# Optimization experiments

Hardware: AMD Instinct MI355X
Metric: run time of the kernel (lower is better)

## Reference

```python
import jax, jax.numpy as jnp
import numpy as np

EPS = 1e-3        # Sinkhorn regularization (SinkhornDistance default)
MAX_ITER = 10     # max Sinkhorn iterations
THRESH = 0.1      # early-stop threshold on |u - u_prev|
N, P, D = 8, 2048, 64


def _l2norm(x):
    # F.normalize(x, dim=-1): x / max(||x||_2, 1e-12)
    return x / jnp.maximum(jnp.linalg.norm(x, axis=-1, keepdims=True), 1e-12)


def _l1norm(x):
    # F.normalize(x, p=1, dim=-1)
    return x / jnp.maximum(jnp.sum(jnp.abs(x), axis=-1, keepdims=True), 1e-12)


def _M(C, u, v):
    # modified cost M_ij = (-C_ij + u_i + v_j) / eps
    return (-C + u[..., :, None] + v[..., None, :]) / EPS


def _sinkhorn_uv(C, mu, nu):
    """Log-domain Sinkhorn with early stopping (matches torch loop + err.item() break)."""
    u0 = jnp.zeros_like(mu)
    v0 = jnp.zeros_like(nu)

    def cond(st):
        i, u, v, err = st
        return jnp.logical_and(i < MAX_ITER, err >= THRESH)

    def body(st):
        i, u, v, _ = st
        u1 = u
        u = EPS * (jnp.log(mu + 1e-8) - jax.nn.logsumexp(_M(C, u, v), axis=-1)) + u
        # logsumexp of M^T over last dim == logsumexp of M over axis -2
        v = EPS * (jnp.log(nu + 1e-8) - jax.nn.logsumexp(_M(C, u, v), axis=-2)) + v
        err = jnp.mean(jnp.sum(jnp.abs(u - u1), axis=-1))
        return (i + 1, u, v, err)

    _, u, v, _ = jax.lax.while_loop(
        cond, body, (jnp.int32(0), u0, v0, jnp.float32(jnp.inf)))
    return u, v


def setup_inputs() -> dict:
    key = jax.random.key(0)
    ka, kb = jax.random.split(key)
    a = jax.random.normal(ka, (N, P, D), dtype=jnp.float32)
    b = jax.random.normal(kb, (N, P, D), dtype=jnp.float32)
    return {"a": a, "b": b}


def reference(a, b):
    a = _l2norm(a)
    b = _l2norm(b)
    cost = 1.0 - jnp.einsum('bnd,bmd->bnm', a, b)          # [N, P1, P2]

    # weights computed from detached cost
    Cd = jax.lax.stop_gradient(cost)
    S = 1.0 - Cd
    wa = _l1norm(jnp.clip(_l1norm(jnp.mean(S, axis=2)), 0.0))  # [N, P1]
    wb = _l1norm(jnp.clip(_l1norm(jnp.mean(S, axis=1)), 0.0))  # [N, P2]

    u, v = _sinkhorn_uv(Cd, wa, wb)
    pi = jax.lax.stop_gradient(jnp.exp(_M(Cd, u, v)))       # transport plan, detached
    D_out = jnp.sum(pi * cost, axis=(-2, -1))               # [N], reduction='none'
    return D_out
```

## Files before the change

### kernel.cpp

```cpp
#include <hip/hip_runtime.h>
#include <math.h>

#define NB 8
#define PP 2048
#define DD 64
#define EPSF 1e-3f
#define RCPE 1000.0f
#define TMAX 10
#define THRESHF 0.1f
#define NEG_INF (-1e30f)
#define QSCALE 32767.5f
#define S_DEQ  (1.0f / 32767.5f)
#define KR 512
#define KC 512
#define TSEL 0.15f
#define TSELQ 4915

typedef __attribute__((ext_vector_type(8))) short bf16x8;
typedef __attribute__((ext_vector_type(4))) float f32x4;

__device__ __forceinline__ float waveAllMax(float v) {
#pragma unroll
    for (int m = 1; m < 64; m <<= 1) v = fmaxf(v, __shfl_xor(v, m, 64));
    return v;
}
__device__ __forceinline__ int waveAllMinI(int v) {
#pragma unroll
    for (int m = 1; m < 64; m <<= 1) v = min(v, __shfl_xor(v, m, 64));
    return v;
}
__device__ __forceinline__ float waveAllSum(float v) {
#pragma unroll
    for (int m = 1; m < 64; m <<= 1) v += __shfl_xor(v, m, 64);
    return v;
}
__device__ __forceinline__ short f2bf(float x) {
    unsigned b = __float_as_uint(x);
    return (short)((b + 0x7FFFu + ((b >> 16) & 1u)) >> 16);
}
__device__ __forceinline__ float bf2f(short h) {
    return __uint_as_float(((unsigned)(unsigned short)h) << 16);
}
__device__ __forceinline__ unsigned pknorm_u16(float a, float b) {
    unsigned r;
    asm("v_cvt_pknorm_u16_f32 %0, %1, %2" : "=v"(r) : "v"(a), "v"(b));
    return r;
}

__global__ void norm_kernel(const float* __restrict__ a, const float* __restrict__ b,
                            short* __restrict__ ahi, short* __restrict__ alo,
                            short* __restrict__ bhi, short* __restrict__ blo,
                            float* __restrict__ u, float* __restrict__ v,
                            int* __restrict__ conv, float* __restrict__ out,
                            float* __restrict__ Sa) {
    int gt = blockIdx.x * 256 + threadIdx.x;
    if (gt < NB * PP) { u[gt] = 0.0f; v[gt] = 0.0f; }
    if (gt == 0) *conv = 0;
    if (gt < NB) out[gt] = 0.0f;
    if (gt < 2 * NB * DD) Sa[gt] = 0.0f;
    int wave = gt >> 6;
    int lane = threadIdx.x & 63;
    const float* src; short* dhi; short* dlo; int row;
    if (wave < NB * PP) { src = a; dhi = ahi; dlo = alo; row = wave; }
    else                { src = b; dhi = bhi; dlo = blo; row = wave - NB * PP; }
    float x = src[(size_t)row * DD + lane];
    float ss = waveAllSum(x * x);
    float r = 1.0f / fmaxf(sqrtf(ss), 1e-12f);
    float xn = x * r;
    short h = f2bf(xn);
    dhi[(size_t)row * DD + lane] = h;
    dlo[(size_t)row * DD + lane] = f2bf(xn - bf2f(h));
}

__global__ void sumvec_kernel(const short* __restrict__ ahi, const short* __restrict__ alo,
                              const short* __restrict__ bhi, const short* __restrict__ blo,
                              float* __restrict__ Sa, float* __restrict__ Sb) {
    int b = blockIdx.x >> 3;
    bool isB = (blockIdx.x >> 2) & 1;
    int qtr = blockIdx.x & 3;
    const short* hi = (isB ? bhi : ahi) + ((size_t)b * PP + qtr * 512) * DD;
    const short* lo = (isB ? blo : alo) + ((size_t)b * PP + qtr * 512) * DD;
    float* dst = (isB ? Sb : Sa) + b * DD;
    int t = threadIdx.x;
    int w = t >> 6, lane = t & 63;
    int rl = lane >> 3, dq = lane & 7;
    float s[8] = {};
#pragma unroll
    for (int it = 0; it < 16; ++it) {
        size_t o = (size_t)(w * 128 + it * 8 + rl) * DD + dq * 8;
        bf16x8 h = *(const bf16x8*)(hi + o);
        bf16x8 l = *(const bf16x8*)(lo + o);
#pragma unroll
        for (int e = 0; e < 8; ++e) s[e] += bf2f(h[e]) + bf2f(l[e]);
    }
#pragma unroll
    for (int e = 0; e < 8; ++e) {
#pragma unroll
        for (int m = 8; m < 64; m <<= 1) s[e] += __shfl_xor(s[e], m, 64);
    }
    __shared__ float sh[4][64];
    if (rl == 0) {
#pragma unroll
        for (int e = 0; e < 8; ++e) sh[w][dq * 8 + e] = s[e];
    }
    __syncthreads();
    if (t < 64) atomicAdd(&dst[t], sh[0][t] + sh[1][t] + sh[2][t] + sh[3][t]);
}

__global__ __launch_bounds__(256, 4) void cost_kernel(const short* __restrict__ ahi,
        const short* __restrict__ alo, const short* __restrict__ bhi,
        const short* __restrict__ blo, unsigned short* __restrict__ C16,
        unsigned* __restrict__ rminp, unsigned* __restrict__ cminp) {
    __shared__ short Bs[2][128 * 64];
    __shared__ unsigned cmin2[4][128];
    int b  = blockIdx.z;
    int i0 = blockIdx.y * 128;
    int j0 = blockIdx.x * 128;
    int t = threadIdx.x, w = t >> 6, lane = t & 63;
    int quad = lane >> 4, li = lane & 15;
    const char* bh = (const char*)(bhi + ((size_t)b * PP + j0) * DD);
    const char* bl = (const char*)(blo + ((size_t)b * PP + j0) * DD);
    uint4 st[8];
#pragma unroll
    for (int i = 0; i < 4; ++i) {
        unsigned x = (unsigned)(t + i * 256) * 16;
        unsigned sx = x ^ (((x >> 7) & 7u) << 4);
        st[i]     = *(const uint4*)(bh + sx);
        st[4 + i] = *(const uint4*)(bl + sx);
    }
#pragma unroll
    for (int i = 0; i < 4; ++i) {
        unsigned x = (unsigned)(t + i * 256) * 16;
        *(uint4*)((char*)&Bs[0][0] + x) = st[i];
        *(uint4*)((char*)&Bs[1][0] + x) = st[4 + i];
    }
    __syncthreads();
    size_t Aoff = ((size_t)b * PP + i0 + w * 32) * DD;
    f32x4 acc[2][2][4] = {};
#pragma unroll
    for (int kc = 0; kc < 2; ++kc) {
        int k0 = kc * 32 + quad * 8;
        bf16x8 fah[2], fal[2];
#pragma unroll
        for (int mt = 0; mt < 2; ++mt) {
            size_t o = Aoff + (size_t)(mt * 16 + li) * DD + k0;
            fah[mt] = *(const bf16x8*)(ahi + o);
            fal[mt] = *(const bf16x8*)(alo + o);
        }
#pragma unroll
        for (int nh = 0; nh < 2; ++nh) {
#pragma unroll
            for (int ntl = 0; ntl < 4; ++ntl) {
                int col = nh * 64 + li * 4 + ntl;
                unsigned xo = ((unsigned)col * 128 + (unsigned)(kc * 4 + quad) * 16)
                              ^ (((unsigned)col & 7u) << 4);
                bf16x8 fbh = *(const bf16x8*)((const char*)&Bs[0][0] + xo);
                bf16x8 fbl = *(const bf16x8*)((const char*)&Bs[1][0] + xo);
#pragma unroll
                for (int mt = 0; mt < 2; ++mt) {
                    acc[mt][nh][ntl] = __builtin_amdgcn_mfma_f32_16x16x32_bf16(
                            fah[mt], fbh, acc[mt][nh][ntl], 0, 0, 0);
                    acc[mt][nh][ntl] = __builtin_amdgcn_mfma_f32_16x16x32_bf16(
                            fah[mt], fbl, acc[mt][nh][ntl], 0, 0, 0);
                    acc[mt][nh][ntl] = __builtin_amdgcn_mfma_f32_16x16x32_bf16(
                            fal[mt], fbh, acc[mt][nh][ntl], 0, 0, 0);
                }
            }
        }
    }
    unsigned cmin[2][4] = {{0xFFFFFFFFu, 0xFFFFFFFFu, 0xFFFFFFFFu, 0xFFFFFFFFu},
                           {0xFFFFFFFFu, 0xFFFFFFFFu, 0xFFFFFFFFu, 0xFFFFFFFFu}};
#pragma unroll
    for (int mt = 0; mt < 2; ++mt) {
#pragma unroll
        for (int r = 0; r < 4; ++r) {
            int irow = w * 32 + mt * 16 + quad * 4 + r;
            unsigned rm = 0xFFFFFFFFu;
            unsigned rowkey = (unsigned)(i0 + irow);
#pragma unroll
            for (int nh = 0; nh < 2; ++nh) {
                float f0 = fmaf(acc[mt][nh][0][r], -0.5f, 0.5f);
                float f1 = fmaf(acc[mt][nh][1][r], -0.5f, 0.5f);
                float f2 = fmaf(acc[mt][nh][2][r], -0.5f, 0.5f);
                float f3 = fmaf(acc[mt][nh][3][r], -0.5f, 0.5f);
                unsigned w0 = pknorm_u16(f0, f1);
                unsigned w1 = pknorm_u16(f2, f3);
                uint2 pv; pv.x = w0; pv.y = w1;
                *(uint2*)&C16[((size_t)b * PP + i0 + irow) * PP + j0 + nh * 64 + li * 4] = pv;
                unsigned colb = (unsigned)(j0 + nh * 64 + li * 4);
                unsigned lo0 = w0 << 16, hi0 = w0 & 0xFFFF0000u;
                unsigned lo1 = w1 << 16, hi1 = w1 & 0xFFFF0000u;
                rm = min(rm, min(min(lo0 | colb, hi0 | (colb + 1)),
                                 min(lo1 | (colb + 2), hi1 | (colb + 3))));
                cmin[nh][0] = min(cmin[nh][0], lo0 | rowkey);
                cmin[nh][1] = min(cmin[nh][1], hi0 | rowkey);
                cmin[nh][2] = min(cmin[nh][2], lo1 | rowkey);
                cmin[nh][3] = min(cmin[nh][3], hi1 | rowkey);
            }
#pragma unroll
            for (int m = 1; m < 16; m <<= 1)
                rm = min(rm, (unsigned)__shfl_xor((int)rm, m, 64));
            if (li == 0)
                rminp[(size_t)blockIdx.x * (NB * PP) + b * PP + i0 + irow] = rm;
        }
    }
#pragma unroll
    for (int nh = 0; nh < 2; ++nh) {
#pragma unroll
        for (int ntl = 0; ntl < 4; ++ntl) {
            unsigned cmv = cmin[nh][ntl];
            cmv = min(cmv, (unsigned)__shfl_xor((int)cmv, 16, 64));
            cmv = min(cmv, (unsigned)__shfl_xor((int)cmv, 32, 64));
            if (quad == 0) cmin2[w][nh * 64 + li * 4 + ntl] = cmv;
        }
    }
    __syncthreads();
    if (t < 128)
        cminp[(size_t)blockIdx.y * (NB * PP) + b * PP + j0 + t] =
            min(min(cmin2[0][t], cmin2[1][t]), min(cmin2[2][t], cmin2[3][t]));
}

__global__ void combine_kernel(const unsigned* __restrict__ rminp,
                               const unsigned* __restrict__ cminp,
                               unsigned* __restrict__ rowminp, unsigned* __restrict__ colminp) {
    int idx = blockIdx.x * 256 + threadIdx.x;
    unsigned rm = 0xFFFFFFFFu, cm = 0xFFFFFFFFu;
#pragma unroll
    for (int k = 0; k < 16; ++k)
        rm = min(rm, rminp[(size_t)k * (NB * PP) + idx]);
#pragma unroll
    for (int k = 0; k < 16; ++k)
        cm = min(cm, cminp[(size_t)k * (NB * PP) + idx]);
    rowminp[idx] = rm; colminp[idx] = cm;
}

__device__ __forceinline__ float blockReduceSum256(float v, float* sh) {
    v = waveAllSum(v);
    int lane = threadIdx.x & 63, w = threadIdx.x >> 6;
    if (lane == 0) sh[w] = v;
    __syncthreads();
    float r = sh[0] + sh[1] + sh[2] + sh[3];
    __syncthreads();
    return r;
}

__global__ void weights_kernel(const float* __restrict__ Sa, const float* __restrict__ Sb,
                               const short* __restrict__ ahi, const short* __restrict__ alo,
                               const short* __restrict__ bhi, const short* __restrict__ blo,
                               const unsigned* __restrict__ rowminp, const unsigned* __restrict__ colminp,
                               float* __restrict__ elm, float* __restrict__ eln,
                               unsigned short* __restrict__ rowminq,
                               unsigned short* __restrict__ colminq,
                               unsigned short* __restrict__ cthq) {
    __shared__ float sh[4];
    __shared__ float sv[64];
    int b = blockIdx.x & 7;
    bool isB = blockIdx.x >= 8;
    const short* hi = (isB ? bhi : ahi) + (size_t)b * PP * DD;
    const short* lo = (isB ? blo : alo) + (size_t)b * PP * DD;
    const float* svecg = (isB ? Sa : Sb) + b * DD;
    float* dst = (isB ? eln : elm) + b * PP;
    int tid = threadIdx.x;
    if (tid < 64) sv[tid] = svecg[tid];
    __syncthreads();
    float x[8];
    float sabs = 0.0f;
#pragma unroll
    for (int q = 0; q < 8; ++q) {
        int row = tid + q * 256;
        float dot = 0.0f;
#pragma unroll
        for (int dq = 0; dq < 8; ++dq) {
            bf16x8 h = *(const bf16x8*)(hi + (size_t)row * DD + dq * 8);
            bf16x8 l = *(const bf16x8*)(lo + (size_t)row * DD + dq * 8);
#pragma unroll
            for (int e = 0; e < 8; ++e)
                dot += (bf2f(h[e]) + bf2f(l[e])) * sv[dq * 8 + e];
        }
        x[q] = dot * (1.0f / (float)PP);
        sabs += fabsf(x[q]);
    }
    sabs = blockReduceSum256(sabs, sh);
    float inv1 = 1.0f / fmaxf(sabs, 1e-12f);
    float spos = 0.0f;
#pragma unroll
    for (int q = 0; q < 8; ++q) {
        x[q] = fmaxf(x[q] * inv1, 0.0f);
        spos += x[q];
    }
    spos = blockReduceSum256(spos, sh);
    float inv2 = 1.0f / fmaxf(spos, 1e-12f);
#pragma unroll
    for (int q = 0; q < 8; ++q)
        dst[tid + q * 256] = EPSF * logf(x[q] * inv2 + 1e-8f);
    if (isB) {
#pragma unroll
        for (int q = 0; q < 8; ++q) {
            int idx = b * PP + tid + q * 256;
            unsigned pc = colminp[idx];
            unsigned arg = pc & 0xffffu;
            unsigned pr = rowminp[b * PP + arg];
            colminq[idx] = (unsigned short)(pc >> 16);
            cthq[idx] = (unsigned short)((pc >> 16) - (pr >> 16));
        }
    } else {
#pragma unroll
        for (int q = 0; q < 8; ++q) {
            int idx = b * PP + tid + q * 256;
            rowminq[idx] = (unsigned short)(rowminp[idx] >> 16);
        }
    }
}

__global__ __launch_bounds__(256) void select_kernel(const unsigned short* __restrict__ C16,
        const unsigned short* __restrict__ colminq, const unsigned short* __restrict__ rowminq,
        const unsigned short* __restrict__ cthq,
        unsigned* __restrict__ rlist, int* __restrict__ rcnt,
        unsigned* __restrict__ clist, int* __restrict__ scnt) {
    __shared__ unsigned tile32[64][36];
    __shared__ int rm_s[64];
    __shared__ unsigned lcnt[64];
    if (blockIdx.x < 4096) {
        int w = threadIdx.x >> 6, lane = threadIdx.x & 63;
        int row = blockIdx.x * 4 + w;
        int b = row >> 11;
        const uint4* cp = (const uint4*)(C16 + (size_t)row * PP);
        uint4 q4[4];
#pragma unroll
        for (int g = 0; g < 4; ++g) q4[g] = cp[g * 64 + lane];
        const unsigned short* cmb = colminq + b * PP;
        int d[32];
        int rpmin = 0x7FFFFFFF;
#pragma unroll
        for (int g = 0; g < 4; ++g) {
            int jb = g * 512 + lane * 8;
            uint4 cmw = *(const uint4*)(cmb + jb);
            unsigned cw[4] = {cmw.x, cmw.y, cmw.z, cmw.w};
            unsigned qq[4] = {q4[g].x, q4[g].y, q4[g].z, q4[g].w};
#pragma unroll
            for (int h = 0; h < 4; ++h) {
                int d0 = (int)(qq[h] & 0xffffu) - (int)(cw[h] & 0xffffu);
                int d1 = (int)(qq[h] >> 16)     - (int)(cw[h] >> 16);
                d[g * 8 + h * 2]     = d0;
                d[g * 8 + h * 2 + 1] = d1;
                rpmin = min(rpmin, min(d0, d1));
            }
        }
        int rth = waveAllMinI(rpmin) + TSELQ;
        int cnt = 0;
#pragma unroll
        for (int e = 0; e < 32; ++e) cnt += (d[e] <= rth) ? 1 : 0;
        int inc = cnt;
#pragma unroll
        for (int m = 1; m < 64; m <<= 1) {
            int t2 = __shfl_up(inc, m, 64);
            if (lane >= m) inc += t2;
        }
        int p = inc - cnt;
        unsigned* rl = rlist + (size_t)row * KR;
#pragma unroll
        for (int g = 0; g < 4; ++g) {
            int jb = g * 512 + lane * 8;
            unsigned qq[4] = {q4[g].x, q4[g].y, q4[g].z, q4[g].w};
#pragma unroll
            for (int e = 0; e < 8; ++e) {
                if (d[g * 8 + e] <= rth) {
                    unsigned q = (qq[e >> 1] >> ((e & 1) * 16)) & 0xffffu;
                    if (p < KR) rl[p] = ((unsigned)(jb + e) << 16) | q;
                    ++p;
                }
            }
        }
        if (lane == 63) rcnt[row] = inc;
    } else {
        int bid = blockIdx.x - 4096;
        int b = bid >> 7;
        int rem = bid & 127;
        int j0 = (rem >> 2) * 64;
        int r0 = (rem & 3) * 512;
        int qq = rem & 3;
        int t = threadIdx.x;
        int col = t & 63, seg = t >> 6;
        int ctj = (int)cthq[b * PP + j0 + col] + TSELQ;
        unsigned* mylist = clist + ((size_t)(b * PP + j0 + col)) * KC + qq * 128;
        if (t < 64) lcnt[t] = 0;
        int lrow = t >> 3, lcc = t & 7;
        uint4 pf0, pf1; int pfr = 0;
        {
            const unsigned short* base0 = C16 + ((size_t)b * PP + r0 + lrow) * PP + j0;
            pf0 = ((const uint4*)base0)[lcc];
            pf1 = ((const uint4*)(base0 + (size_t)32 * PP))[lcc];
            if (t < 64) pfr = (int)rowminq[b * PP + r0 + t];
        }
        for (int chunk = 0; chunk < 8; ++chunk) {
            *(uint4*)&tile32[lrow][lcc * 4]      = pf0;
            *(uint4*)&tile32[32 + lrow][lcc * 4] = pf1;
            if (t < 64) rm_s[t] = pfr;
            __syncthreads();
            if (chunk < 7) {
                int rn = r0 + (chunk + 1) * 64;
                const unsigned short* base0 = C16 + ((size_t)b * PP + rn + lrow) * PP + j0;
                pf0 = ((const uint4*)base0)[lcc];
                pf1 = ((const uint4*)(base0 + (size_t)32 * PP))[lcc];
                if (t < 64) pfr = (int)rowminq[b * PP + rn + t];
            }
            int rbase = r0 + chunk * 64;
            unsigned qv[16];
            unsigned mask16 = 0;
            int sel = 0;
#pragma unroll
            for (int rr = 0; rr < 16; ++rr) {
                int rowl = seg * 16 + rr;
                unsigned w32 = tile32[rowl][col >> 1];
                unsigned q = (col & 1) ? (w32 >> 16) : (w32 & 0xffffu);
                qv[rr] = q;
                if ((int)q - rm_s[rowl] <= ctj) { mask16 |= 1u << rr; ++sel; }
            }
            unsigned basep = sel ? atomicAdd(&lcnt[col], (unsigned)sel) : 0u;
#pragma unroll
            for (int rr = 0; rr < 16; ++rr) {
                if (mask16 & (1u << rr)) {
                    if (basep < 128)
                        mylist[basep] = ((unsigned)(rbase + seg * 16 + rr) << 16) | qv[rr];
                    ++basep;
                }
            }
            __syncthreads();
        }
        if (t < 64)
            scnt[(b * PP + j0 + t) * 4 + qq] = min((int)lcnt[t], 128);
    }
}

__global__ __launch_bounds__(512) void u_kernel(const unsigned* __restrict__ rlist,
        const int* __restrict__ rcnt, const float* __restrict__ v,
        const float* __restrict__ elm, float* __restrict__ u, float* __restrict__ du,
        const int* __restrict__ conv) {
    if (*conv) return;
    int g = threadIdx.x >> 4, l = threadIdx.x & 15;
    int row = blockIdx.x * 32 + g;
    int b = row >> 11;
    int cnt = min(rcnt[row], KR);
    const unsigned* lst = rlist + (size_t)row * KR;
    const float* vb = v + (b << 11);
    float m = NEG_INF;
    for (int e = l; e < cnt; e += 16) {
        unsigned wd = lst[e];
        m = fmaxf(m, vb[wd >> 16] - (float)(wd & 0xffffu) * S_DEQ);
    }
#pragma unroll
    for (int mm = 1; mm < 16; mm <<= 1) m = fmaxf(m, __shfl_xor(m, mm, 64));
    float s = 0.0f;
    for (int e = l; e < cnt; e += 16) {
        unsigned wd = lst[e];
        float x = vb[wd >> 16] - (float)(wd & 0xffffu) * S_DEQ;
        s += __expf((x - m) * RCPE);
    }
#pragma unroll
    for (int mm = 1; mm < 16; mm <<= 1) s += __shfl_xor(s, mm, 64);
    if (l == 0) {
        float un = elm[row] - m - EPSF * logf(s);
        du[row] = fabsf(un - u[row]);
        u[row] = un;
    }
}

__global__ __launch_bounds__(512) void v_kernel(const unsigned* __restrict__ clist,
        const int* __restrict__ scnt, const float* __restrict__ u,
        const float* __restrict__ eln, float* __restrict__ v,
        const float* __restrict__ du, int* __restrict__ conv) {
    if (*conv) return;
    int g = threadIdx.x >> 4, l = threadIdx.x & 15;
    int jg = blockIdx.x * 32 + g;
    int b = jg >> 11;
    int4 sc = *(const int4*)&scnt[jg * 4];
    int cn[4] = {sc.x, sc.y, sc.z, sc.w};
    const unsigned* lst = clist + (size_t)jg * KC;
    const float* ub = u + (b << 11);
    float m = NEG_INF;
#pragma unroll
    for (int sg = 0; sg < 4; ++sg) {
        for (int k = l; k < cn[sg]; k += 16) {
            unsigned wd = lst[sg * 128 + k];
            m = fmaxf(m, ub[wd >> 16] - (float)(wd & 0xffffu) * S_DEQ);
        }
    }
#pragma unroll
    for (int mm = 1; mm < 16; mm <<= 1) m = fmaxf(m, __shfl_xor(m, mm, 64));
    float s = 0.0f;
#pragma unroll
    for (int sg = 0; sg < 4; ++sg) {
        for (int k = l; k < cn[sg]; k += 16) {
            unsigned wd = lst[sg * 128 + k];
            float x = ub[wd >> 16] - (float)(wd & 0xffffu) * S_DEQ;
            s += __expf((x - m) * RCPE);
        }
    }
#pragma unroll
    for (int mm = 1; mm < 16; mm <<= 1) s += __shfl_xor(s, mm, 64);
    if (l == 0)
        v[jg] = eln[jg] - m - EPSF * logf(s);
    if (blockIdx.x == 0) {
        __shared__ float sh[8];
        int t = threadIdx.x;
        int w = t >> 6, lane = t & 63;
        float sacc = 0.0f;
#pragma unroll
        for (int q = 0; q < 32; ++q) sacc += du[t + q * 512];
        sacc = waveAllSum(sacc);
        if (lane == 0) sh[w] = sacc;
        __syncthreads();
        if (t == 0) {
            float tot = sh[0] + sh[1] + sh[2] + sh[3] + sh[4] + sh[5] + sh[6] + sh[7];
            if (tot * (1.0f / (float)NB) < THRESHF) *conv = 1;
        }
    }
}

__global__ __launch_bounds__(512) void emd_kernel(const unsigned* __restrict__ rlist,
        const int* __restrict__ rcnt, const float* __restrict__ u,
        const float* __restrict__ v, float* __restrict__ epart) {
    __shared__ float sh[8];
    int g = threadIdx.x >> 4, l = threadIdx.x & 15;
    int row = blockIdx.x * 32 + g;
    int b = row >> 11;
    int cnt = min(rcnt[row], KR);
    const unsigned* lst = rlist + (size_t)row * KR;
    const float* vb = v + (b << 11);
    float ui = u[row];
    float s = 0.0f;
    for (int e = l; e < cnt; e += 16) {
        unsigned wd = lst[e];
        float cf = (float)(wd & 0xffffu) * S_DEQ;
        s += __expf((ui + vb[wd >> 16] - cf) * RCPE) * cf;
    }
    s = waveAllSum(s);
    int w = threadIdx.x >> 6, lane = threadIdx.x & 63;
    if (lane == 0) sh[w] = s;
    __syncthreads();
    if (threadIdx.x == 0)
        epart[blockIdx.x] = sh[0] + sh[1] + sh[2] + sh[3] + sh[4] + sh[5] + sh[6] + sh[7];
}

__global__ void emd_finalize(const float* __restrict__ epart,
                             float* __restrict__ out) {
    int b = blockIdx.x, l = threadIdx.x;
    float s = epart[b * 64 + l];
    s = waveAllSum(s);
    if (l == 0) out[b] = s;
}

extern "C" void kernel_launch(void* const* d_in, const int* in_sizes, int n_in,
                              void* d_out, int out_size, void* d_ws, size_t ws_size,
                              hipStream_t stream) {
    const float* a = (const float*)d_in[0];
    const float* b = (const float*)d_in[1];
    float* out = (float*)d_out;

    const size_t MBs = 1024ull * 1024ull;
    char* ws = (char*)d_ws;
    unsigned short* C16 = (unsigned short*)ws;
    short* ahi   = (short*)(ws + 64 * MBs);
    short* alo   = (short*)(ws + 66 * MBs);
    short* bhi   = (short*)(ws + 68 * MBs);
    short* blo   = (short*)(ws + 70 * MBs);
    unsigned* rminp = (unsigned*)(ws + 72 * MBs);
    unsigned* cminp = (unsigned*)(ws + 74 * MBs);
    unsigned* rlist = (unsigned*)(ws + 64 * MBs);
    unsigned* clist = (unsigned*)(ws + 96 * MBs);
    char* tail = ws + 128 * MBs;
    size_t off = 0;
    const size_t szV = (size_t)NB * PP * 4;
    const size_t szH = (size_t)NB * PP * 2;
    int*   scnt    = (int*)(tail + off); off += (size_t)NB * PP * 4 * 4;
    unsigned* rowminp = (unsigned*)(tail + off); off += szV;
    unsigned* colminp = (unsigned*)(tail + off); off += szV;
    unsigned short* rowminq = (unsigned short*)(tail + off); off += szH;
    unsigned short* colminq = (unsigned short*)(tail + off); off += szH;
    unsigned short* cthq    = (unsigned short*)(tail + off); off += szH;
    float* elm     = (float*)(tail + off); off += szV;
    float* eln     = (float*)(tail + off); off += szV;
    float* u       = (float*)(tail + off); off += szV;
    float* v       = (float*)(tail + off); off += szV;
    float* du      = (float*)(tail + off); off += szV;
    int*   rcnt    = (int*)(tail + off); off += szV;
    float* Sa      = (float*)(tail + off); off += (size_t)2 * NB * DD * 4;
    float* Sb      = Sa + NB * DD;
    float* epart   = (float*)(tail + off); off += (size_t)512 * 4;
    int*   conv    = (int*)(tail + off); off += 64;
    if (ws_size < 128 * MBs + off) return;

    norm_kernel<<<(2 * NB * PP) / 4, 256, 0, stream>>>(a, b, ahi, alo, bhi, blo,
            u, v, conv, out, Sa);
    sumvec_kernel<<<64, 256, 0, stream>>>(ahi, alo, bhi, blo, Sa, Sb);
    cost_kernel<<<dim3(PP / 128, PP / 128, NB), 256, 0, stream>>>(
            ahi, alo, bhi, blo, C16, rminp, cminp);
    combine_kernel<<<64, 256, 0, stream>>>(rminp, cminp, rowminp, colminp);
    weights_kernel<<<16, 256, 0, stream>>>(Sa, Sb, ahi, alo, bhi, blo,
            rowminp, colminp, elm, eln, rowminq, colminq, cthq);
    select_kernel<<<4096 + 1024, 256, 0, stream>>>(C16, colminq, rowminq,
            cthq, rlist, rcnt, clist, scnt);
    for (int it = 0; it < TMAX; ++it) {
        u_kernel<<<NB * PP / 32, 512, 0, stream>>>(rlist, rcnt, v, elm, u, du, conv);
        v_kernel<<<NB * PP / 32, 512, 0, stream>>>(clist, scnt, u, eln, v, du, conv);
    }
    emd_kernel<<<NB * PP / 32, 512, 0, stream>>>(rlist, rcnt, u, v, epart);
    emd_finalize<<<NB, 64, 0, stream>>>(epart, out);
}
```

Before: 351.1 us.

## Fuse Sinkhorn iterations and EMD into one persistent kernel with grid barriers

Replaces the 20 separate u/v kernel launches plus the EMD and finalize kernels with a single persistent kernel of 128 blocks. The blocks synchronize through atomic-counter grid barriers, and convergence is checked in-kernel so the loop exits early. The aim is to remove per-launch overhead and the idle tail of many small kernels. In exchange, only 128 blocks run, each handling 4 rows per 16-lane group, so parallelism drops. Spin barriers also rely on all blocks being co-resident.

```diff
diff --git a/kernel.cpp b/kernel.cpp
--- a/kernel.cpp
+++ b/kernel.cpp
@@ -15,6 +15,7 @@
 #define KC 512
 #define TSEL 0.15f
 #define TSELQ 4915
+#define SBLK 128
 
 typedef __attribute__((ext_vector_type(8))) short bf16x8;
 typedef __attribute__((ext_vector_type(4))) float f32x4;
@@ -45,6 +46,18 @@
     unsigned r;
     asm("v_cvt_pknorm_u16_f32 %0, %1, %2" : "=v"(r) : "v"(a), "v"(b));
     return r;
+}
+__device__ __forceinline__ void gridBarrier(int* cnt, int target) {
+    __syncthreads();
+    if (threadIdx.x == 0) {
+        __threadfence();
+        atomicAdd(cnt, 1);
+        while (__hip_atomic_load(cnt, __ATOMIC_RELAXED,
+                                 __HIP_MEMORY_SCOPE_AGENT) < target)
+            __builtin_amdgcn_s_sleep(8);
+        __threadfence();
+    }
+    __syncthreads();
 }
 
 __global__ void norm_kernel(const float* __restrict__ a, const float* __restrict__ b,
@@ -52,12 +65,13 @@
                             short* __restrict__ bhi, short* __restrict__ blo,
                             float* __restrict__ u, float* __restrict__ v,
                             int* __restrict__ conv, float* __restrict__ out,
-                            float* __restrict__ Sa) {
+                            float* __restrict__ Sa, int* __restrict__ bars) {
     int gt = blockIdx.x * 256 + threadIdx.x;
     if (gt < NB * PP) { u[gt] = 0.0f; v[gt] = 0.0f; }
     if (gt == 0) *conv = 0;
     if (gt < NB) out[gt] = 0.0f;
     if (gt < 2 * NB * DD) Sa[gt] = 0.0f;
+    if (gt < 64) bars[gt] = 0;
     int wave = gt >> 6;
     int lane = threadIdx.x & 63;
     const float* src; short* dhi; short* dlo; int row;
@@ -432,122 +446,124 @@
     }
 }
 
-__global__ __launch_bounds__(512) void u_kernel(const unsigned* __restrict__ rlist,
-        const int* __restrict__ rcnt, const float* __restrict__ v,
-        const float* __restrict__ elm, float* __restrict__ u, float* __restrict__ du,
-        const int* __restrict__ conv) {
-    if (*conv) return;
-    int g = threadIdx.x >> 4, l = threadIdx.x & 15;
-    int row = blockIdx.x * 32 + g;
-    int b = row >> 11;
-    int cnt = min(rcnt[row], KR);
-    const unsigned* lst = rlist + (size_t)row * KR;
-    const float* vb = v + (b << 11);
-    float m = NEG_INF;
-    for (int e = l; e < cnt; e += 16) {
-        unsigned wd = lst[e];
-        m = fmaxf(m, vb[wd >> 16] - (float)(wd & 0xffffu) * S_DEQ);
-    }
-#pragma unroll
-    for (int mm = 1; mm < 16; mm <<= 1) m = fmaxf(m, __shfl_xor(m, mm, 64));
+__global__ __launch_bounds__(512) void sinkhorn_kernel(
+        const unsigned* __restrict__ rlist, const int* __restrict__ rcnt,
+        const unsigned* __restrict__ clist, const int* __restrict__ scnt,
+        const float* __restrict__ elm, const float* __restrict__ eln,
+        float* __restrict__ u, float* __restrict__ v,
+        float* __restrict__ du, float* __restrict__ epart,
+        float* __restrict__ out, int* __restrict__ conv, int* __restrict__ bars) {
+    int t = threadIdx.x;
+    int g = t >> 4, l = t & 15;
+    int blk = blockIdx.x;
+    int bi = 0;
+    __shared__ float sh[8];
+    for (int it = 0; it < TMAX; ++it) {
+#pragma unroll
+        for (int k = 0; k < 4; ++k) {
+            int row = blk * 128 + g * 4 + k;
+            int b = row >> 11;
+            int cnt = min(rcnt[row], KR);
+            const unsigned* lst = rlist + (size_t)row * KR;
+            const float* vb = v + (b << 11);
+            float m = NEG_INF;
+            for (int e = l; e < cnt; e += 16) {
+                unsigned wd = lst[e];
+                m = fmaxf(m, vb[wd >> 16] - (float)(wd & 0xffffu) * S_DEQ);
+            }
+#pragma unroll
+            for (int mm = 1; mm < 16; mm <<= 1) m = fmaxf(m, __shfl_xor(m, mm, 64));
+            float s = 0.0f;
+            for (int e = l; e < cnt; e += 16) {
+                unsigned wd = lst[e];
+                s += __expf((vb[wd >> 16] - (float)(wd & 0xffffu) * S_DEQ - m) * RCPE);
+            }
+#pragma unroll
+            for (int mm = 1; mm < 16; mm <<= 1) s += __shfl_xor(s, mm, 64);
+            if (l == 0) {
+                float un = elm[row] - m - EPSF * logf(s);
+                du[row] = fabsf(un - u[row]);
+                u[row] = un;
+            }
+        }
+        gridBarrier(&bars[bi++], SBLK);
+        if (blk == 0) {
+            float sacc = 0.0f;
+#pragma unroll
+            for (int q = 0; q < 32; ++q) sacc += du[t + q * 512];
+            sacc = waveAllSum(sacc);
+            if ((t & 63) == 0) sh[t >> 6] = sacc;
+            __syncthreads();
+            if (t == 0) {
+                float tot = sh[0] + sh[1] + sh[2] + sh[3] + sh[4] + sh[5] + sh[6] + sh[7];
+                if (tot * (1.0f / (float)NB) < THRESHF)
+                    __hip_atomic_store(conv, 1, __ATOMIC_RELAXED,
+                                       __HIP_MEMORY_SCOPE_AGENT);
+            }
+            __syncthreads();
+        }
+#pragma unroll
+        for (int k = 0; k < 4; ++k) {
+            int jg = blk * 128 + g * 4 + k;
+            int b = jg >> 11;
+            int4 sc = *(const int4*)&scnt[jg * 4];
+            int cn[4] = {sc.x, sc.y, sc.z, sc.w};
+            const unsigned* lst = clist + (size_t)jg * KC;
+            const float* ub = u + (b << 11);
+            float m = NEG_INF;
+#pragma unroll
+            for (int sg = 0; sg < 4; ++sg) {
+                for (int kk = l; kk < cn[sg]; kk += 16) {
+                    unsigned wd = lst[sg * 128 + kk];
+                    m = fmaxf(m, ub[wd >> 16] - (float)(wd & 0xffffu) * S_DEQ);
+                }
+            }
+#pragma unroll
+            for (int mm = 1; mm < 16; mm <<= 1) m = fmaxf(m, __shfl_xor(m, mm, 64));
+            float s = 0.0f;
+#pragma unroll
+            for (int sg = 0; sg < 4; ++sg) {
+                for (int kk = l; kk < cn[sg]; kk += 16) {
+                    unsigned wd = lst[sg * 128 + kk];
+                    s += __expf((ub[wd >> 16] - (float)(wd & 0xffffu) * S_DEQ - m) * RCPE);
+                }
+            }
+#pragma unroll
+            for (int mm = 1; mm < 16; mm <<= 1) s += __shfl_xor(s, mm, 64);
+            if (l == 0)
+                v[jg] = eln[jg] - m - EPSF * logf(s);
+        }
+        gridBarrier(&bars[bi++], SBLK);
+        if (__hip_atomic_load(conv, __ATOMIC_RELAXED, __HIP_MEMORY_SCOPE_AGENT))
+            break;
+    }
     float s = 0.0f;
-    for (int e = l; e < cnt; e += 16) {
-        unsigned wd = lst[e];
-        float x = vb[wd >> 16] - (float)(wd & 0xffffu) * S_DEQ;
-        s += __expf((x - m) * RCPE);
-    }
-#pragma unroll
-    for (int mm = 1; mm < 16; mm <<= 1) s += __shfl_xor(s, mm, 64);
-    if (l == 0) {
-        float un = elm[row] - m - EPSF * logf(s);
-        du[row] = fabsf(un - u[row]);
-        u[row] = un;
-    }
-}
-
-__global__ __launch_bounds__(512) void v_kernel(const unsigned* __restrict__ clist,
-        const int* __restrict__ scnt, const float* __restrict__ u,
-        const float* __restrict__ eln, float* __restrict__ v,
-        const float* __restrict__ du, int* __restrict__ conv) {
-    if (*conv) return;
-    int g = threadIdx.x >> 4, l = threadIdx.x & 15;
-    int jg = blockIdx.x * 32 + g;
-    int b = jg >> 11;
-    int4 sc = *(const int4*)&scnt[jg * 4];
-    int cn[4] = {sc.x, sc.y, sc.z, sc.w};
-    const unsigned* lst = clist + (size_t)jg * KC;
-    const float* ub = u + (b << 11);
-    float m = NEG_INF;
-#pragma unroll
-    for (int sg = 0; sg < 4; ++sg) {
-        for (int k = l; k < cn[sg]; k += 16) {
-            unsigned wd = lst[sg * 128 + k];
-            m = fmaxf(m, ub[wd >> 16] - (float)(wd & 0xffffu) * S_DEQ);
-        }
-    }
-#pragma unroll
-    for (int mm = 1; mm < 16; mm <<= 1) m = fmaxf(m, __shfl_xor(m, mm, 64));
-    float s = 0.0f;
-#pragma unroll
-    for (int sg = 0; sg < 4; ++sg) {
-        for (int k = l; k < cn[sg]; k += 16) {
-            unsigned wd = lst[sg * 128 + k];
-            float x = ub[wd >> 16] - (float)(wd & 0xffffu) * S_DEQ;
-            s += __expf((x - m) * RCPE);
-        }
-    }
-#pragma unroll
-    for (int mm = 1; mm < 16; mm <<= 1) s += __shfl_xor(s, mm, 64);
-    if (l == 0)
-        v[jg] = eln[jg] - m - EPSF * logf(s);
-    if (blockIdx.x == 0) {
-        __shared__ float sh[8];
-        int t = threadIdx.x;
-        int w = t >> 6, lane = t & 63;
-        float sacc = 0.0f;
-#pragma unroll
-        for (int q = 0; q < 32; ++q) sacc += du[t + q * 512];
-        sacc = waveAllSum(sacc);
-        if (lane == 0) sh[w] = sacc;
-        __syncthreads();
-        if (t == 0) {
-            float tot = sh[0] + sh[1] + sh[2] + sh[3] + sh[4] + sh[5] + sh[6] + sh[7];
-            if (tot * (1.0f / (float)NB) < THRESHF) *conv = 1;
-        }
-    }
-}
-
-__global__ __launch_bounds__(512) void emd_kernel(const unsigned* __restrict__ rlist,
-        const int* __restrict__ rcnt, const float* __restrict__ u,
-        const float* __restrict__ v, float* __restrict__ epart) {
-    __shared__ float sh[8];
-    int g = threadIdx.x >> 4, l = threadIdx.x & 15;
-    int row = blockIdx.x * 32 + g;
-    int b = row >> 11;
-    int cnt = min(rcnt[row], KR);
-    const unsigned* lst = rlist + (size_t)row * KR;
-    const float* vb = v + (b << 11);
-    float ui = u[row];
-    float s = 0.0f;
-    for (int e = l; e < cnt; e += 16) {
-        unsigned wd = lst[e];
-        float cf = (float)(wd & 0xffffu) * S_DEQ;
-        s += __expf((ui + vb[wd >> 16] - cf) * RCPE) * cf;
+#pragma unroll
+    for (int k = 0; k < 4; ++k) {
+        int row = blk * 128 + g * 4 + k;
+        int b = row >> 11;
+        int cnt = min(rcnt[row], KR);
+        const unsigned* lst = rlist + (size_t)row * KR;
+        const float* vb = v + (b << 11);
+        float ui = u[row];
+        for (int e = l; e < cnt; e += 16) {
+            unsigned wd = lst[e];
+            float cf = (float)(wd & 0xffffu) * S_DEQ;
+            s += __expf((ui + vb[wd >> 16] - cf) * RCPE) * cf;
+        }
     }
     s = waveAllSum(s);
-    int w = threadIdx.x >> 6, lane = threadIdx.x & 63;
-    if (lane == 0) sh[w] = s;
-    __syncthreads();
-    if (threadIdx.x == 0)
-        epart[blockIdx.x] = sh[0] + sh[1] + sh[2] + sh[3] + sh[4] + sh[5] + sh[6] + sh[7];
-}
-
-__global__ void emd_finalize(const float* __restrict__ epart,
-                             float* __restrict__ out) {
-    int b = blockIdx.x, l = threadIdx.x;
-    float s = epart[b * 64 + l];
-    s = waveAllSum(s);
-    if (l == 0) out[b] = s;
+    if ((t & 63) == 0) sh[t >> 6] = s;
+    __syncthreads();
+    if (t == 0)
+        epart[blk] = sh[0] + sh[1] + sh[2] + sh[3] + sh[4] + sh[5] + sh[6] + sh[7];
+    gridBarrier(&bars[bi++], SBLK);
+    if (blk == 0 && t < 128) {
+        float e = epart[t];
+#pragma unroll
+        for (int mm = 1; mm < 16; mm <<= 1) e += __shfl_xor(e, mm, 64);
+        if ((t & 15) == 0) out[t >> 4] = e;
+    }
 }
 
 extern "C" void kernel_launch(void* const* d_in, const int* in_sizes, int n_in,
@@ -586,12 +602,13 @@
     int*   rcnt    = (int*)(tail + off); off += szV;
     float* Sa      = (float*)(tail + off); off += (size_t)2 * NB * DD * 4;
     float* Sb      = Sa + NB * DD;
-    float* epart   = (float*)(tail + off); off += (size_t)512 * 4;
+    float* epart   = (float*)(tail + off); off += (size_t)SBLK * 4;
     int*   conv    = (int*)(tail + off); off += 64;
+    int*   bars    = (int*)(tail + off); off += 64 * 4;
     if (ws_size < 128 * MBs + off) return;
 
     norm_kernel<<<(2 * NB * PP) / 4, 256, 0, stream>>>(a, b, ahi, alo, bhi, blo,
-            u, v, conv, out, Sa);
+            u, v, conv, out, Sa, bars);
     sumvec_kernel<<<64, 256, 0, stream>>>(ahi, alo, bhi, blo, Sa, Sb);
     cost_kernel<<<dim3(PP / 128, PP / 128, NB), 256, 0, stream>>>(
             ahi, alo, bhi, blo, C16, rminp, cminp);
@@ -600,10 +617,6 @@
             rowminp, colminp, elm, eln, rowminq, colminq, cthq);
     select_kernel<<<4096 + 1024, 256, 0, stream>>>(C16, colminq, rowminq,
             cthq, rlist, rcnt, clist, scnt);
-    for (int it = 0; it < TMAX; ++it) {
-        u_kernel<<<NB * PP / 32, 512, 0, stream>>>(rlist, rcnt, v, elm, u, du, conv);
-        v_kernel<<<NB * PP / 32, 512, 0, stream>>>(clist, scnt, u, eln, v, du, conv);
-    }
-    emd_kernel<<<NB * PP / 32, 512, 0, stream>>>(rlist, rcnt, u, v, epart);
-    emd_finalize<<<NB, 64, 0, stream>>>(epart, out);
-}
+    sinkhorn_kernel<<<SBLK, 512, 0, stream>>>(rlist, rcnt, clist, scnt,
+            elm, eln, u, v, du, epart, out, conv, bars);
+}
```

Result: slower. 778.2 us (+121.6%).

## Fuse sumvec, combine and finalize stages into neighbouring kernels to cut launches

Applied to the files above, without the earlier changes.

The separate column-sum kernel is removed: norm_kernel now writes per-block partial sums of the normalized rows, and weights_kernel reduces them. The combine kernel that min-reduces the 16 partial row and column minima is folded into weights_kernel, using shared memory for the row-min lookup. emd_finalize is dropped in favour of atomicAdd into the output, with each emd block covering two row groups. This removes three kernel launches and their dependency bubbles, but it puts more serial reduction work into the 16-block weights kernel and adds float atomics.

```diff
diff --git a/kernel.cpp b/kernel.cpp
--- a/kernel.cpp
+++ b/kernel.cpp
@@ -52,13 +52,14 @@
                             short* __restrict__ bhi, short* __restrict__ blo,
                             float* __restrict__ u, float* __restrict__ v,
                             int* __restrict__ conv, float* __restrict__ out,
-                            float* __restrict__ Sa) {
+                            float* __restrict__ svpart) {
+    __shared__ float shn[4][64];
     int gt = blockIdx.x * 256 + threadIdx.x;
     if (gt < NB * PP) { u[gt] = 0.0f; v[gt] = 0.0f; }
     if (gt == 0) *conv = 0;
     if (gt < NB) out[gt] = 0.0f;
-    if (gt < 2 * NB * DD) Sa[gt] = 0.0f;
     int wave = gt >> 6;
+    int wl = threadIdx.x >> 6;
     int lane = threadIdx.x & 63;
     const float* src; short* dhi; short* dlo; int row;
     if (wave < NB * PP) { src = a; dhi = ahi; dlo = alo; row = wave; }
@@ -70,41 +71,12 @@
     short h = f2bf(xn);
     dhi[(size_t)row * DD + lane] = h;
     dlo[(size_t)row * DD + lane] = f2bf(xn - bf2f(h));
-}
-
-__global__ void sumvec_kernel(const short* __restrict__ ahi, const short* __restrict__ alo,
-                              const short* __restrict__ bhi, const short* __restrict__ blo,
-                              float* __restrict__ Sa, float* __restrict__ Sb) {
-    int b = blockIdx.x >> 3;
-    bool isB = (blockIdx.x >> 2) & 1;
-    int qtr = blockIdx.x & 3;
-    const short* hi = (isB ? bhi : ahi) + ((size_t)b * PP + qtr * 512) * DD;
-    const short* lo = (isB ? blo : alo) + ((size_t)b * PP + qtr * 512) * DD;
-    float* dst = (isB ? Sb : Sa) + b * DD;
-    int t = threadIdx.x;
-    int w = t >> 6, lane = t & 63;
-    int rl = lane >> 3, dq = lane & 7;
-    float s[8] = {};
-#pragma unroll
-    for (int it = 0; it < 16; ++it) {
-        size_t o = (size_t)(w * 128 + it * 8 + rl) * DD + dq * 8;
-        bf16x8 h = *(const bf16x8*)(hi + o);
-        bf16x8 l = *(const bf16x8*)(lo + o);
-#pragma unroll
-        for (int e = 0; e < 8; ++e) s[e] += bf2f(h[e]) + bf2f(l[e]);
-    }
-#pragma unroll
-    for (int e = 0; e < 8; ++e) {
-#pragma unroll
-        for (int m = 8; m < 64; m <<= 1) s[e] += __shfl_xor(s[e], m, 64);
-    }
-    __shared__ float sh[4][64];
-    if (rl == 0) {
-#pragma unroll
-        for (int e = 0; e < 8; ++e) sh[w][dq * 8 + e] = s[e];
-    }
-    __syncthreads();
-    if (t < 64) atomicAdd(&dst[t], sh[0][t] + sh[1][t] + sh[2][t] + sh[3][t]);
+    shn[wl][lane] = xn;
+    __syncthreads();
+    if (threadIdx.x < 64)
+        svpart[(size_t)blockIdx.x * 64 + threadIdx.x] =
+            shn[0][threadIdx.x] + shn[1][threadIdx.x] +
+            shn[2][threadIdx.x] + shn[3][threadIdx.x];
 }
 
 __global__ __launch_bounds__(256, 4) void cost_kernel(const short* __restrict__ ahi,
@@ -220,20 +192,6 @@
             min(min(cmin2[0][t], cmin2[1][t]), min(cmin2[2][t], cmin2[3][t]));
 }
 
-__global__ void combine_kernel(const unsigned* __restrict__ rminp,
-                               const unsigned* __restrict__ cminp,
-                               unsigned* __restrict__ rowminp, unsigned* __restrict__ colminp) {
-    int idx = blockIdx.x * 256 + threadIdx.x;
-    unsigned rm = 0xFFFFFFFFu, cm = 0xFFFFFFFFu;
-#pragma unroll
-    for (int k = 0; k < 16; ++k)
-        rm = min(rm, rminp[(size_t)k * (NB * PP) + idx]);
-#pragma unroll
-    for (int k = 0; k < 16; ++k)
-        cm = min(cm, cminp[(size_t)k * (NB * PP) + idx]);
-    rowminp[idx] = rm; colminp[idx] = cm;
-}
-
 __device__ __forceinline__ float blockReduceSum256(float v, float* sh) {
     v = waveAllSum(v);
     int lane = threadIdx.x & 63, w = threadIdx.x >> 6;
@@ -244,25 +202,69 @@
     return r;
 }
 
-__global__ void weights_kernel(const float* __restrict__ Sa, const float* __restrict__ Sb,
+__global__ void weights_kernel(const float* __restrict__ svpart,
                                const short* __restrict__ ahi, const short* __restrict__ alo,
                                const short* __restrict__ bhi, const short* __restrict__ blo,
-                               const unsigned* __restrict__ rowminp, const unsigned* __restrict__ colminp,
+                               const unsigned* __restrict__ rminp, const unsigned* __restrict__ cminp,
                                float* __restrict__ elm, float* __restrict__ eln,
                                unsigned short* __restrict__ rowminq,
                                unsigned short* __restrict__ colminq,
                                unsigned short* __restrict__ cthq) {
     __shared__ float sh[4];
+    __shared__ float shred[4][64];
     __shared__ float sv[64];
+    __shared__ int rowmin_s[PP];
     int b = blockIdx.x & 7;
     bool isB = blockIdx.x >= 8;
     const short* hi = (isB ? bhi : ahi) + (size_t)b * PP * DD;
     const short* lo = (isB ? blo : alo) + (size_t)b * PP * DD;
-    const float* svecg = (isB ? Sa : Sb) + b * DD;
     float* dst = (isB ? eln : elm) + b * PP;
     int tid = threadIdx.x;
-    if (tid < 64) sv[tid] = svecg[tid];
-    __syncthreads();
+    int w = tid >> 6, lane = tid & 63;
+    {
+        int base = isB ? (b * 512) : (4096 + b * 512);
+        float acc = 0.0f;
+#pragma unroll 4
+        for (int k = 0; k < 128; ++k)
+            acc += svpart[(size_t)(base + w * 128 + k) * 64 + lane];
+        shred[w][lane] = acc;
+    }
+    __syncthreads();
+    if (tid < 64)
+        sv[tid] = shred[0][tid] + shred[1][tid] + shred[2][tid] + shred[3][tid];
+    if (isB) {
+        for (int r = tid; r < PP; r += 256) {
+            unsigned rm = 0xFFFFFFFFu;
+#pragma unroll
+            for (int s = 0; s < 16; ++s)
+                rm = min(rm, rminp[(size_t)s * (NB * PP) + b * PP + r]);
+            rowmin_s[r] = (int)(rm >> 16);
+        }
+        __syncthreads();
+#pragma unroll
+        for (int q = 0; q < 8; ++q) {
+            int c = tid + q * 256;
+            int idx = b * PP + c;
+            unsigned cm = 0xFFFFFFFFu;
+#pragma unroll
+            for (int s = 0; s < 16; ++s)
+                cm = min(cm, cminp[(size_t)s * (NB * PP) + idx]);
+            colminq[idx] = (unsigned short)(cm >> 16);
+            cthq[idx] = (unsigned short)((int)(cm >> 16) - rowmin_s[cm & 0xffffu]);
+        }
+    } else {
+        __syncthreads();
+#pragma unroll
+        for (int q = 0; q < 8; ++q) {
+            int r = tid + q * 256;
+            int idx = b * PP + r;
+            unsigned rm = 0xFFFFFFFFu;
+#pragma unroll
+            for (int s = 0; s < 16; ++s)
+                rm = min(rm, rminp[(size_t)s * (NB * PP) + idx]);
+            rowminq[idx] = (unsigned short)(rm >> 16);
+        }
+    }
     float x[8];
     float sabs = 0.0f;
 #pragma unroll
@@ -293,23 +295,6 @@
 #pragma unroll
     for (int q = 0; q < 8; ++q)
         dst[tid + q * 256] = EPSF * logf(x[q] * inv2 + 1e-8f);
-    if (isB) {
-#pragma unroll
-        for (int q = 0; q < 8; ++q) {
-            int idx = b * PP + tid + q * 256;
-            unsigned pc = colminp[idx];
-            unsigned arg = pc & 0xffffu;
-            unsigned pr = rowminp[b * PP + arg];
-            colminq[idx] = (unsigned short)(pc >> 16);
-            cthq[idx] = (unsigned short)((pc >> 16) - (pr >> 16));
-        }
-    } else {
-#pragma unroll
-        for (int q = 0; q < 8; ++q) {
-            int idx = b * PP + tid + q * 256;
-            rowminq[idx] = (unsigned short)(rowminp[idx] >> 16);
-        }
-    }
 }
 
 __global__ __launch_bounds__(256) void select_kernel(const unsigned short* __restrict__ C16,
@@ -519,35 +504,30 @@
 
 __global__ __launch_bounds__(512) void emd_kernel(const unsigned* __restrict__ rlist,
         const int* __restrict__ rcnt, const float* __restrict__ u,
-        const float* __restrict__ v, float* __restrict__ epart) {
+        const float* __restrict__ v, float* __restrict__ out) {
     __shared__ float sh[8];
     int g = threadIdx.x >> 4, l = threadIdx.x & 15;
-    int row = blockIdx.x * 32 + g;
-    int b = row >> 11;
-    int cnt = min(rcnt[row], KR);
-    const unsigned* lst = rlist + (size_t)row * KR;
+    int b = blockIdx.x >> 5;
     const float* vb = v + (b << 11);
-    float ui = u[row];
     float s = 0.0f;
-    for (int e = l; e < cnt; e += 16) {
-        unsigned wd = lst[e];
-        float cf = (float)(wd & 0xffffu) * S_DEQ;
-        s += __expf((ui + vb[wd >> 16] - cf) * RCPE) * cf;
+#pragma unroll
+    for (int k = 0; k < 2; ++k) {
+        int row = blockIdx.x * 64 + k * 32 + g;
+        int cnt = min(rcnt[row], KR);
+        const unsigned* lst = rlist + (size_t)row * KR;
+        float ui = u[row];
+        for (int e = l; e < cnt; e += 16) {
+            unsigned wd = lst[e];
+            float cf = (float)(wd & 0xffffu) * S_DEQ;
+            s += __expf((ui + vb[wd >> 16] - cf) * RCPE) * cf;
+        }
     }
     s = waveAllSum(s);
     int w = threadIdx.x >> 6, lane = threadIdx.x & 63;
     if (lane == 0) sh[w] = s;
     __syncthreads();
     if (threadIdx.x == 0)
-        epart[blockIdx.x] = sh[0] + sh[1] + sh[2] + sh[3] + sh[4] + sh[5] + sh[6] + sh[7];
-}
-
-__global__ void emd_finalize(const float* __restrict__ epart,
-                             float* __restrict__ out) {
-    int b = blockIdx.x, l = threadIdx.x;
-    float s = epart[b * 64 + l];
-    s = waveAllSum(s);
-    if (l == 0) out[b] = s;
+        atomicAdd(&out[b], sh[0] + sh[1] + sh[2] + sh[3] + sh[4] + sh[5] + sh[6] + sh[7]);
 }
 
 extern "C" void kernel_launch(void* const* d_in, const int* in_sizes, int n_in,
@@ -565,7 +545,8 @@
     short* bhi   = (short*)(ws + 68 * MBs);
     short* blo   = (short*)(ws + 70 * MBs);
     unsigned* rminp = (unsigned*)(ws + 72 * MBs);
-    unsigned* cminp = (unsigned*)(ws + 74 * MBs);
+    unsigned* cminp = (unsigned*)(ws + 73 * MBs);
+    float* svpart  = (float*)(ws + 74 * MBs);
     unsigned* rlist = (unsigned*)(ws + 64 * MBs);
     unsigned* clist = (unsigned*)(ws + 96 * MBs);
     char* tail = ws + 128 * MBs;
@@ -573,8 +554,6 @@
     const size_t szV = (size_t)NB * PP * 4;
     const size_t szH = (size_t)NB * PP * 2;
     int*   scnt    = (int*)(tail + off); off += (size_t)NB * PP * 4 * 4;
-    unsigned* rowminp = (unsigned*)(tail + off); off += szV;
-    unsigned* colminp = (unsigned*)(tail + off); off += szV;
     unsigned short* rowminq = (unsigned short*)(tail + off); off += szH;
     unsigned short* colminq = (unsigned short*)(tail + off); off += szH;
     unsigned short* cthq    = (unsigned short*)(tail + off); off += szH;
@@ -584,26 +563,20 @@
     float* v       = (float*)(tail + off); off += szV;
     float* du      = (float*)(tail + off); off += szV;
     int*   rcnt    = (int*)(tail + off); off += szV;
-    float* Sa      = (float*)(tail + off); off += (size_t)2 * NB * DD * 4;
-    float* Sb      = Sa + NB * DD;
-    float* epart   = (float*)(tail + off); off += (size_t)512 * 4;
     int*   conv    = (int*)(tail + off); off += 64;
     if (ws_size < 128 * MBs + off) return;
 
     norm_kernel<<<(2 * NB * PP) / 4, 256, 0, stream>>>(a, b, ahi, alo, bhi, blo,
-            u, v, conv, out, Sa);
-    sumvec_kernel<<<64, 256, 0, stream>>>(ahi, alo, bhi, blo, Sa, Sb);
+            u, v, conv, out, svpart);
     cost_kernel<<<dim3(PP / 128, PP / 128, NB), 256, 0, stream>>>(
             ahi, alo, bhi, blo, C16, rminp, cminp);
-    combine_kernel<<<64, 256, 0, stream>>>(rminp, cminp, rowminp, colminp);
-    weights_kernel<<<16, 256, 0, stream>>>(Sa, Sb, ahi, alo, bhi, blo,
-            rowminp, colminp, elm, eln, rowminq, colminq, cthq);
+    weights_kernel<<<16, 256, 0, stream>>>(svpart, ahi, alo, bhi, blo,
+            rminp, cminp, elm, eln, rowminq, colminq, cthq);
     select_kernel<<<4096 + 1024, 256, 0, stream>>>(C16, colminq, rowminq,
             cthq, rlist, rcnt, clist, scnt);
     for (int it = 0; it < TMAX; ++it) {
         u_kernel<<<NB * PP / 32, 512, 0, stream>>>(rlist, rcnt, v, elm, u, du, conv);
         v_kernel<<<NB * PP / 32, 512, 0, stream>>>(clist, scnt, u, eln, v, du, conv);
     }
-    emd_kernel<<<NB * PP / 32, 512, 0, stream>>>(rlist, rcnt, u, v, epart);
-    emd_finalize<<<NB, 64, 0, stream>>>(epart, out);
-}
+    emd_kernel<<<NB * PP / 64, 512, 0, stream>>>(rlist, rcnt, u, v, out);
+}
```

Result: slower. 358.7 us (+2.2%).
